# Optimization experiments

Measured on AMD Instinct MI355X. Metric: run time of the kernel, lower is better.

## Reference

```python
import jax, jax.numpy as jnp
import numpy as np

EPS = 1e-5  # torch default for InstanceNorm2d and BatchNorm2d
B, C, H, W = 16, 128, 8192, 1


def _instance_norm(x):
    # normalize over spatial dims (H, W) per sample, per channel; affine=False (torch default)
    mean = jnp.mean(x, axis=(2, 3), keepdims=True)
    var = jnp.var(x, axis=(2, 3), keepdims=True)
    return (x - mean) * jax.lax.rsqrt(var + EPS)


def _batch_norm(x, gamma, beta):
    # training-mode batch norm: stats over (B, H, W) per channel, affine transform
    mean = jnp.mean(x, axis=(0, 2, 3), keepdims=True)
    var = jnp.var(x, axis=(0, 2, 3), keepdims=True)
    xn = (x - mean) * jax.lax.rsqrt(var + EPS)
    return xn * gamma[None, :, None, None] + beta[None, :, None, None]


def _block(x, g, be, w, b):
    # InstanceNorm -> BatchNorm -> ReLU -> 1x1 Conv
    x = jax.nn.relu(_batch_norm(_instance_norm(x), g, be))
    return jnp.einsum('bchw,oc->bohw', x, w) + b[None, :, None, None]


def setup_inputs() -> dict:
    key = jax.random.key(0)
    ks = jax.random.split(key, 6)
    return {
        'Correlation_feats': jax.random.normal(ks[0], (B, C, H, W), jnp.float32),
        'Coherence_residual_feats': jax.random.normal(ks[1], (B, C, H, W), jnp.float32),
        'feats': jax.random.normal(ks[2], (B, C, H, W), jnp.float32),
        'fc_w': jax.random.normal(ks[3], (2 * C,), jnp.float32) * 0.05,
        'fc_b': jnp.zeros((1,), jnp.float32),
        'w1': jax.random.normal(ks[4], (C, C), jnp.float32) * (1.0 / np.sqrt(C)),
        'b1': jnp.zeros((C,), jnp.float32),
        'g1': jnp.ones((C,), jnp.float32),
        'be1': jnp.zeros((C,), jnp.float32),
        'w2': jax.random.normal(ks[5], (C, C), jnp.float32) * (1.0 / np.sqrt(C)),
        'b2': jnp.zeros((C,), jnp.float32),
        'g2': jnp.ones((C,), jnp.float32),
        'be2': jnp.zeros((C,), jnp.float32),
    }


def reference(Correlation_feats, Coherence_residual_feats, feats,
              fc_w, fc_b, w1, b1, g1, be1, w2, b2, g2, be2):
    # pre_defined_alpha is None branch: alpha = sigmoid(fc(cat(Corr, Coh)))
    cat = jnp.concatenate([Correlation_feats, Coherence_residual_feats], axis=1)  # [B,2C,H,W]
    logit = jnp.einsum('bchw,c->bhw', cat, fc_w)[:, None, :, :] + fc_b[0]  # [B,1,H,W]
    alpha = jax.nn.sigmoid(logit)
    agg = Correlation_feats - alpha * feats
    x = _block(agg, g1, be1, w1, b1)
    x = _block(x, g2, be2, w2, b2)
    return x
```

## Files before the change

### kernel.cpp

```cpp
#include <hip/hip_runtime.h>

#define NB 16
#define NC 128
#define NH 8192
#define EPSN 1e-5f

typedef __attribute__((ext_vector_type(8))) short short8;
typedef __attribute__((ext_vector_type(4))) float f32x4;

__device__ inline unsigned short f2bf(float f) {
  unsigned int u = __builtin_bit_cast(unsigned int, f);
  u = u + 0x7FFFu + ((u >> 16) & 1u);
  return (unsigned short)(u >> 16);
}
__device__ inline float bf2f(unsigned short h) {
  unsigned int u = ((unsigned int)h) << 16;
  return __builtin_bit_cast(float, u);
}

__global__ __launch_bounds__(256, 4) void alpha_kernel(
    const float* __restrict__ corr, const float* __restrict__ coh,
    const float* __restrict__ fcw, const float* __restrict__ fcb,
    float* __restrict__ alpha) {
  __shared__ float part[8][128];
  const int t = threadIdx.x;
  const int b = blockIdx.x >> 6;
  const int h0 = (blockIdx.x & 63) << 7;
  const int cg = t >> 5;
  const int quad = t & 31;

  const float* pc = corr + ((size_t)(b * NC + cg * 8) << 13) + h0 + quad * 4;
  const float* ph = coh + ((size_t)(b * NC + cg * 8) << 13) + h0 + quad * 4;

  float fw0[8], fw1[8], fw2[8], fw3[8];
#pragma unroll
  for (int k = 0; k < 2; ++k) {
    *(float4*)&fw0[k * 4] = *(const float4*)(fcw + cg * 8 + k * 4);
    *(float4*)&fw1[k * 4] = *(const float4*)(fcw + 64 + cg * 8 + k * 4);
    *(float4*)&fw2[k * 4] = *(const float4*)(fcw + 128 + cg * 8 + k * 4);
    *(float4*)&fw3[k * 4] = *(const float4*)(fcw + 192 + cg * 8 + k * 4);
  }

  float4 xa[8], xb[8], xc[8], xd[8];
#pragma unroll
  for (int j = 0; j < 8; ++j) xa[j] = *(const float4*)(pc + ((size_t)j << 13));
#pragma unroll
  for (int j = 0; j < 8; ++j)
    xb[j] = *(const float4*)(pc + ((size_t)(64 + j) << 13));

  float4 acc0 = {0, 0, 0, 0}, acc1 = {0, 0, 0, 0};
#pragma unroll
  for (int j = 0; j < 8; ++j) xc[j] = *(const float4*)(ph + ((size_t)j << 13));
#pragma unroll
  for (int j = 0; j < 8; ++j) {
    acc0.x = fmaf(xa[j].x, fw0[j], acc0.x);
    acc0.y = fmaf(xa[j].y, fw0[j], acc0.y);
    acc0.z = fmaf(xa[j].z, fw0[j], acc0.z);
    acc0.w = fmaf(xa[j].w, fw0[j], acc0.w);
  }
#pragma unroll
  for (int j = 0; j < 8; ++j)
    xd[j] = *(const float4*)(ph + ((size_t)(64 + j) << 13));
#pragma unroll
  for (int j = 0; j < 8; ++j) {
    acc1.x = fmaf(xb[j].x, fw1[j], acc1.x);
    acc1.y = fmaf(xb[j].y, fw1[j], acc1.y);
    acc1.z = fmaf(xb[j].z, fw1[j], acc1.z);
    acc1.w = fmaf(xb[j].w, fw1[j], acc1.w);
  }
#pragma unroll
  for (int j = 0; j < 8; ++j) {
    acc0.x = fmaf(xc[j].x, fw2[j], acc0.x);
    acc0.y = fmaf(xc[j].y, fw2[j], acc0.y);
    acc0.z = fmaf(xc[j].z, fw2[j], acc0.z);
    acc0.w = fmaf(xc[j].w, fw2[j], acc0.w);
  }
#pragma unroll
  for (int j = 0; j < 8; ++j) {
    acc1.x = fmaf(xd[j].x, fw3[j], acc1.x);
    acc1.y = fmaf(xd[j].y, fw3[j], acc1.y);
    acc1.z = fmaf(xd[j].z, fw3[j], acc1.z);
    acc1.w = fmaf(xd[j].w, fw3[j], acc1.w);
  }

  float4 s;
  s.x = acc0.x + acc1.x;
  s.y = acc0.y + acc1.y;
  s.z = acc0.z + acc1.z;
  s.w = acc0.w + acc1.w;
  *(float4*)&part[cg][quad * 4] = s;
  __syncthreads();
  if (t < 128) {
    float l = fcb[0];
#pragma unroll
    for (int pidx = 0; pidx < 8; ++pidx) l += part[pidx][t];
    alpha[b * NH + h0 + t] = 1.0f / (1.0f + __expf(-l));
  }
}

__global__ __launch_bounds__(256) void agg_kernel(
    const float* __restrict__ corr, const float* __restrict__ feats,
    const float* __restrict__ alpha, float* __restrict__ agg,
    float* __restrict__ stats) {
  int blk = blockIdx.x;
  int chunk = blk & 3;
  int bc = blk >> 2;
  int b = bc >> 7;
  size_t base = (size_t)bc * NH + chunk * 2048;
  const float* pa = alpha + (size_t)b * NH + chunk * 2048;
  int t = threadIdx.x;
  float s = 0.f, q = 0.f;
#pragma unroll
  for (int r = 0; r < 2; ++r) {
    int off = r * 1024 + t * 4;
    float4 cv = *(const float4*)(corr + base + off);
    float4 fv = *(const float4*)(feats + base + off);
    float4 av = *(const float4*)(pa + off);
    float4 g;
    g.x = cv.x - av.x * fv.x;
    g.y = cv.y - av.y * fv.y;
    g.z = cv.z - av.z * fv.z;
    g.w = cv.w - av.w * fv.w;
    *(float4*)(agg + base + off) = g;
    s += (g.x + g.y) + (g.z + g.w);
    q = fmaf(g.x, g.x, q);
    q = fmaf(g.y, g.y, q);
    q = fmaf(g.z, g.z, q);
    q = fmaf(g.w, g.w, q);
  }
#pragma unroll
  for (int m = 32; m >= 1; m >>= 1) {
    s += __shfl_xor(s, m);
    q += __shfl_xor(q, m);
  }
  __shared__ float red[8];
  int wid = t >> 6;
  if ((t & 63) == 0) {
    red[wid * 2] = s;
    red[wid * 2 + 1] = q;
  }
  __syncthreads();
  if (t == 0) {
    float S = (red[0] + red[2]) + (red[4] + red[6]);
    float Q = (red[1] + red[3]) + (red[5] + red[7]);
    atomicAdd(&stats[bc * 2], S);
    atomicAdd(&stats[bc * 2 + 1], Q);
  }
}

__global__ void finalize_kernel(const float* __restrict__ stats,
                                const float* __restrict__ g,
                                const float* __restrict__ be,
                                float* __restrict__ scale,
                                float* __restrict__ shift) {
  int c = threadIdx.x;
  float mean[NB], rstd[NB];
  float bnacc = 0.f;
#pragma unroll
  for (int b = 0; b < NB; ++b) {
    float s = stats[(b * NC + c) * 2];
    float q = stats[(b * NC + c) * 2 + 1];
    float m = s * (1.f / NH);
    float v = fmaxf(q * (1.f / NH) - m * m, 0.f);
    float r = rsqrtf(v + EPSN);
    mean[b] = m;
    rstd[b] = r;
    bnacc += v * r * r;
  }
  float bnr = rsqrtf(bnacc * (1.f / NB) + EPSN);
  float gc = g[c], bec = be[c];
#pragma unroll
  for (int b = 0; b < NB; ++b) {
    float sc = rstd[b] * bnr * gc;
    scale[b * NC + c] = sc;
    shift[b * NC + c] = fmaf(-mean[b], sc, bec);
  }
}

template <bool INBF, bool OUTBF, bool DOSTATS>
__global__ __launch_bounds__(256) void conv_mfma_kernel(
    const void* Xv, const float* __restrict__ scale,
    const float* __restrict__ shift, const float* __restrict__ W,
    const float* __restrict__ bias, void* Outv, float* __restrict__ stats) {
  __shared__ __align__(16) unsigned short sXf[8192];
  __shared__ float ssum[NC], ssq[NC];
  const int t = threadIdx.x;
  const int b = blockIdx.x >> 6;
  const int hbase = (blockIdx.x & 63) << 7;
  const int lane = t & 63;
  const int wv = t >> 6;
  const int wo = wv >> 1;
  const int wh = wv & 1;

  if (DOSTATS && t < NC) { ssum[t] = 0.f; ssq[t] = 0.f; }

  const int cb = (t >> 4) << 3;
  const int hq = t & 15;
  const int fragw = ((hq >> 2) << 2) + (cb >> 5);
  const int sub0 = (((cb >> 3) & 3) << 4) + ((hq & 3) << 2);
  const unsigned swz = ((unsigned)(sub0 >> 3)) << 4;
  const unsigned br = ((unsigned)(lane << 4)) ^ (((unsigned)(lane >> 3)) << 4);

  const float* Xf = (const float*)Xv;
  const unsigned short* Xh = (const unsigned short*)Xv;
  float* Of = (float*)Outv;
  unsigned short* Oh = (unsigned short*)Outv;

  float4 xv[8];
#pragma unroll
  for (int p = 0; p < 8; ++p) {
    size_t idx = ((size_t)(b * NC + cb + p) << 13) + hbase + hq * 4;
    if (INBF) {
      ushort4 u = *(const ushort4*)(Xh + idx);
      xv[p] = make_float4(bf2f(u.x), bf2f(u.y), bf2f(u.z), bf2f(u.w));
    } else {
      xv[p] = *(const float4*)(Xf + idx);
    }
  }

  float scv[8], shv[8];
#pragma unroll
  for (int p = 0; p < 8; ++p) {
    scv[p] = scale[b * NC + cb + p];
    shv[p] = shift[b * NC + cb + p];
  }

  short8 wfr[4][4];
  {
    const int orow = wo * 64 + (lane & 15);
    const int cbw = 8 * (lane >> 4);
#pragma unroll
    for (int m = 0; m < 4; ++m) {
#pragma unroll
      for (int k = 0; k < 4; ++k) {
        const float* p = W + (orow + m * 16) * NC + k * 32 + cbw;
        float4 lo = *(const float4*)p;
        float4 hi = *(const float4*)(p + 4);
        union { short8 s; unsigned short u[8]; } fr;
        fr.u[0] = f2bf(lo.x); fr.u[1] = f2bf(lo.y);
        fr.u[2] = f2bf(lo.z); fr.u[3] = f2bf(lo.w);
        fr.u[4] = f2bf(hi.x); fr.u[5] = f2bf(hi.y);
        fr.u[6] = f2bf(hi.z); fr.u[7] = f2bf(hi.w);
        wfr[m][k] = fr.s;
      }
    }
  }

  float as_[4][4], aq_[4][4];
  if (DOSTATS) {
#pragma unroll
    for (int m = 0; m < 4; ++m)
#pragma unroll
      for (int r = 0; r < 4; ++r) { as_[m][r] = 0.f; aq_[m][r] = 0.f; }
  }

  const int og = (lane >> 4) << 2;
  const int hcol = lane & 15;

  for (int tt = 0; tt < 2; ++tt) {
#pragma unroll
    for (int r = 0; r < 4; ++r) {
      union { short8 s; unsigned short u[8]; } pk;
#pragma unroll
      for (int p = 0; p < 8; ++p) {
        float v = (r == 0) ? xv[p].x : (r == 1) ? xv[p].y : (r == 2) ? xv[p].z : xv[p].w;
        pk.u[p] = f2bf(fmaxf(fmaf(v, scv[p], shv[p]), 0.f));
      }
      unsigned addr = ((unsigned)(fragw << 10)) + ((((unsigned)(sub0 + r)) << 4) ^ swz);
      *(short8*)((char*)sXf + addr) = pk.s;
    }
    if (tt < 1) {
#pragma unroll
      for (int p = 0; p < 8; ++p) {
        size_t idx = ((size_t)(b * NC + cb + p) << 13) + hbase + 64 + hq * 4;
        if (INBF) {
          ushort4 u = *(const ushort4*)(Xh + idx);
          xv[p] = make_float4(bf2f(u.x), bf2f(u.y), bf2f(u.z), bf2f(u.w));
        } else {
          xv[p] = *(const float4*)(Xf + idx);
        }
      }
    }
    __syncthreads();

    f32x4 acc[4][2];
#pragma unroll
    for (int m = 0; m < 4; ++m) {
      acc[m][0] = (f32x4){0.f, 0.f, 0.f, 0.f};
      acc[m][1] = (f32x4){0.f, 0.f, 0.f, 0.f};
    }
#pragma unroll
    for (int k = 0; k < 4; ++k) {
      short8 x0 = *(const short8*)((char*)sXf + (((wh * 2 + 0) * 4 + k) << 10) + br);
      short8 x1 = *(const short8*)((char*)sXf + (((wh * 2 + 1) * 4 + k) << 10) + br);
#pragma unroll
      for (int m = 0; m < 4; ++m) {
        acc[m][0] = __builtin_amdgcn_mfma_f32_16x16x32_bf16(wfr[m][k], x0, acc[m][0], 0, 0, 0);
        acc[m][1] = __builtin_amdgcn_mfma_f32_16x16x32_bf16(wfr[m][k], x1, acc[m][1], 0, 0, 0);
      }
    }

    const int ha = hbase + tt * 64 + wh * 32 + hcol;
#pragma unroll
    for (int m = 0; m < 4; ++m) {
      int obase = wo * 64 + m * 16 + og;
#pragma unroll
      for (int r = 0; r < 4; ++r) {
        int o = obase + r;
        float bv = bias[o];
        float v0 = acc[m][0][r] + bv;
        float v1 = acc[m][1][r] + bv;
        size_t ob = ((size_t)(b * NC + o) << 13);
        if (OUTBF) {
          Oh[ob + ha] = f2bf(v0);
          Oh[ob + ha + 16] = f2bf(v1);
        } else {
          Of[ob + ha] = v0;
          Of[ob + ha + 16] = v1;
        }
        if (DOSTATS) {
          as_[m][r] += v0 + v1;
          aq_[m][r] = fmaf(v0, v0, fmaf(v1, v1, aq_[m][r]));
        }
      }
    }
    __syncthreads();
  }

  if (DOSTATS) {
#pragma unroll
    for (int m = 0; m < 4; ++m) {
#pragma unroll
      for (int r = 0; r < 4; ++r) {
        float s = as_[m][r], q = aq_[m][r];
#pragma unroll
        for (int mm = 1; mm <= 8; mm <<= 1) {
          s += __shfl_xor(s, mm);
          q += __shfl_xor(q, mm);
        }
        if (hcol == 0) {
          int o = wo * 64 + m * 16 + og + r;
          atomicAdd(&ssum[o], s);
          atomicAdd(&ssq[o], q);
        }
      }
    }
    __syncthreads();
    if (t < NC) {
      atomicAdd(&stats[(b * NC + t) * 2], ssum[t]);
      atomicAdd(&stats[(b * NC + t) * 2 + 1], ssq[t]);
    }
  }
}

extern "C" void kernel_launch(void* const* d_in, const int* in_sizes, int n_in,
                              void* d_out, int out_size, void* d_ws,
                              size_t ws_size, hipStream_t stream) {
  const float* corr = (const float*)d_in[0];
  const float* coh = (const float*)d_in[1];
  const float* feats = (const float*)d_in[2];
  const float* fcw = (const float*)d_in[3];
  const float* fcb = (const float*)d_in[4];
  const float* w1 = (const float*)d_in[5];
  const float* b1 = (const float*)d_in[6];
  const float* g1 = (const float*)d_in[7];
  const float* be1 = (const float*)d_in[8];
  const float* w2 = (const float*)d_in[9];
  const float* b2 = (const float*)d_in[10];
  const float* g2 = (const float*)d_in[11];
  const float* be2 = (const float*)d_in[12];

  float* out = (float*)d_out;
  float* ws = (float*)d_ws;
  float* alphab = ws;
  float* stats1 = alphab + 131072;
  float* stats2 = stats1 + 4096;
  float* scale1 = stats2 + 4096;
  float* shift1 = scale1 + 2048;
  float* scale2 = shift1 + 2048;
  float* shift2 = scale2 + 2048;
  const size_t small_floats = 131072 + 4096 + 4096 + 4 * 2048;
  unsigned short* x1h = (unsigned short*)(ws + small_floats);
  const size_t need = small_floats * sizeof(float) +
                      (size_t)NB * NC * NH * sizeof(unsigned short);

  hipMemsetAsync(stats1, 0, 8192 * sizeof(float), stream);
  alpha_kernel<<<1024, 256, 0, stream>>>(corr, coh, fcw, fcb, alphab);
  agg_kernel<<<8192, 256, 0, stream>>>(corr, feats, alphab, out, stats1);
  finalize_kernel<<<1, 128, 0, stream>>>(stats1, g1, be1, scale1, shift1);

  if (ws_size >= need) {
    conv_mfma_kernel<false, true, true><<<1024, 256, 0, stream>>>(
        out, scale1, shift1, w1, b1, x1h, stats2);
    finalize_kernel<<<1, 128, 0, stream>>>(stats2, g2, be2, scale2, shift2);
    conv_mfma_kernel<true, false, false><<<1024, 256, 0, stream>>>(
        x1h, scale2, shift2, w2, b2, out, nullptr);
  } else {
    conv_mfma_kernel<false, false, true><<<1024, 256, 0, stream>>>(
        out, scale1, shift1, w1, b1, out, stats2);
    finalize_kernel<<<1, 128, 0, stream>>>(stats2, g2, be2, scale2, shift2);
    conv_mfma_kernel<false, false, false><<<1024, 256, 0, stream>>>(
        out, scale2, shift2, w2, b2, out, nullptr);
  }
}
```

Measured before the change: 132.7 us.

## Rewrite alpha kernel with double-buffered direct global-to-LDS channel loads

After: 143.9 us. +8.5%, slower.

```diff
diff --git a/kernel.cpp b/kernel.cpp
--- a/kernel.cpp
+++ b/kernel.cpp
@@ -18,84 +18,54 @@
   return __builtin_bit_cast(float, u);
 }
 
-__global__ __launch_bounds__(256, 4) void alpha_kernel(
+__global__ __launch_bounds__(256) void alpha_kernel(
     const float* __restrict__ corr, const float* __restrict__ coh,
     const float* __restrict__ fcw, const float* __restrict__ fcb,
     float* __restrict__ alpha) {
-  __shared__ float part[8][128];
+  __shared__ __align__(16) float sbuf[2][4096];
   const int t = threadIdx.x;
-  const int b = blockIdx.x >> 6;
-  const int h0 = (blockIdx.x & 63) << 7;
-  const int cg = t >> 5;
-  const int quad = t & 31;
-
-  const float* pc = corr + ((size_t)(b * NC + cg * 8) << 13) + h0 + quad * 4;
-  const float* ph = coh + ((size_t)(b * NC + cg * 8) << 13) + h0 + quad * 4;
-
-  float fw0[8], fw1[8], fw2[8], fw3[8];
-#pragma unroll
-  for (int k = 0; k < 2; ++k) {
-    *(float4*)&fw0[k * 4] = *(const float4*)(fcw + cg * 8 + k * 4);
-    *(float4*)&fw1[k * 4] = *(const float4*)(fcw + 64 + cg * 8 + k * 4);
-    *(float4*)&fw2[k * 4] = *(const float4*)(fcw + 128 + cg * 8 + k * 4);
-    *(float4*)&fw3[k * 4] = *(const float4*)(fcw + 192 + cg * 8 + k * 4);
-  }
-
-  float4 xa[8], xb[8], xc[8], xd[8];
-#pragma unroll
-  for (int j = 0; j < 8; ++j) xa[j] = *(const float4*)(pc + ((size_t)j << 13));
-#pragma unroll
-  for (int j = 0; j < 8; ++j)
-    xb[j] = *(const float4*)(pc + ((size_t)(64 + j) << 13));
-
-  float4 acc0 = {0, 0, 0, 0}, acc1 = {0, 0, 0, 0};
-#pragma unroll
-  for (int j = 0; j < 8; ++j) xc[j] = *(const float4*)(ph + ((size_t)j << 13));
-#pragma unroll
-  for (int j = 0; j < 8; ++j) {
-    acc0.x = fmaf(xa[j].x, fw0[j], acc0.x);
-    acc0.y = fmaf(xa[j].y, fw0[j], acc0.y);
-    acc0.z = fmaf(xa[j].z, fw0[j], acc0.z);
-    acc0.w = fmaf(xa[j].w, fw0[j], acc0.w);
-  }
-#pragma unroll
-  for (int j = 0; j < 8; ++j)
-    xd[j] = *(const float4*)(ph + ((size_t)(64 + j) << 13));
-#pragma unroll
-  for (int j = 0; j < 8; ++j) {
-    acc1.x = fmaf(xb[j].x, fw1[j], acc1.x);
-    acc1.y = fmaf(xb[j].y, fw1[j], acc1.y);
-    acc1.z = fmaf(xb[j].z, fw1[j], acc1.z);
-    acc1.w = fmaf(xb[j].w, fw1[j], acc1.w);
-  }
-#pragma unroll
-  for (int j = 0; j < 8; ++j) {
-    acc0.x = fmaf(xc[j].x, fw2[j], acc0.x);
-    acc0.y = fmaf(xc[j].y, fw2[j], acc0.y);
-    acc0.z = fmaf(xc[j].z, fw2[j], acc0.z);
-    acc0.w = fmaf(xc[j].w, fw2[j], acc0.w);
-  }
-#pragma unroll
-  for (int j = 0; j < 8; ++j) {
-    acc1.x = fmaf(xd[j].x, fw3[j], acc1.x);
-    acc1.y = fmaf(xd[j].y, fw3[j], acc1.y);
-    acc1.z = fmaf(xd[j].z, fw3[j], acc1.z);
-    acc1.w = fmaf(xd[j].w, fw3[j], acc1.w);
-  }
-
-  float4 s;
-  s.x = acc0.x + acc1.x;
-  s.y = acc0.y + acc1.y;
-  s.z = acc0.z + acc1.z;
-  s.w = acc0.w + acc1.w;
-  *(float4*)&part[cg][quad * 4] = s;
-  __syncthreads();
-  if (t < 128) {
-    float l = fcb[0];
-#pragma unroll
-    for (int pidx = 0; pidx < 8; ++pidx) l += part[pidx][t];
-    alpha[b * NH + h0 + t] = 1.0f / (1.0f + __expf(-l));
-  }
+  const int b = blockIdx.x >> 5;
+  const int h0 = (blockIdx.x & 31) << 8;
+  const int w = t >> 6;
+  const int lane = t & 63;
+
+#define STAGE(BUFIDX, K)                                                       \
+  {                                                                            \
+    const float* src_ = ((K) < 8) ? corr : coh;                                \
+    const float* g_ = src_ +                                                   \
+                      ((size_t)(b * NC + (((K) & 7) * 16) + 4 * w) << 13) +    \
+                      h0 + lane * 4;                                           \
+    _Pragma("unroll") for (int r_ = 0; r_ < 4; ++r_) {                         \
+      __builtin_amdgcn_global_load_lds(                                        \
+          (const __attribute__((address_space(1))) void*)(g_ +                 \
+                                                          ((size_t)r_ << 13)), \
+          (__attribute__((address_space(3))) void*)&sbuf[BUFIDX]               \
+                                                        [(4 * w + r_) * 256],  \
+          16, 0, 0);                                                           \
+    }                                                                          \
+  }
+
+  STAGE(0, 0);
+  float acc0 = 0.f, acc1 = 0.f;
+  for (int k = 0; k < 16; ++k) {
+    if (k < 15) STAGE((k + 1) & 1, k + 1);
+    __syncthreads();
+    float wreg[16];
+#pragma unroll
+    for (int q = 0; q < 4; ++q)
+      *(float4*)&wreg[q * 4] = *(const float4*)(fcw + k * 16 + q * 4);
+    const float* bufc = &sbuf[k & 1][0];
+#pragma unroll
+    for (int j = 0; j < 16; j += 2) {
+      acc0 = fmaf(bufc[j * 256 + t], wreg[j], acc0);
+      acc1 = fmaf(bufc[(j + 1) * 256 + t], wreg[j + 1], acc1);
+    }
+    __syncthreads();
+  }
+#undef STAGE
+
+  float l = acc0 + acc1 + fcb[0];
+  alpha[b * NH + h0 + t] = 1.0f / (1.0f + __expf(-l));
 }
 
 __global__ __launch_bounds__(256) void agg_kernel(
@@ -385,7 +355,7 @@
                       (size_t)NB * NC * NH * sizeof(unsigned short);
 
   hipMemsetAsync(stats1, 0, 8192 * sizeof(float), stream);
-  alpha_kernel<<<1024, 256, 0, stream>>>(corr, coh, fcw, fcb, alphab);
+  alpha_kernel<<<512, 256, 0, stream>>>(corr, coh, fcw, fcb, alphab);
   agg_kernel<<<8192, 256, 0, stream>>>(corr, feats, alphab, out, stats1);
   finalize_kernel<<<1, 128, 0, stream>>>(stats1, g1, be1, scale1, shift1);
 
```

## Split alpha logit computation into channel-partitioned partial sums plus reduction kernel

Applied to the files above, without the earlier changes.

Result: slower. 137.0 us (+3.3%).

```diff
diff --git a/kernel.cpp b/kernel.cpp
--- a/kernel.cpp
+++ b/kernel.cpp
@@ -18,7 +18,56 @@
   return __builtin_bit_cast(float, u);
 }
 
-__global__ __launch_bounds__(256, 4) void alpha_kernel(
+__global__ __launch_bounds__(256) void alpha_part_kernel(
+    const float* __restrict__ corr, const float* __restrict__ coh,
+    const float* __restrict__ fcw, float* __restrict__ partial) {
+  const int t = threadIdx.x;
+  const int blk = blockIdx.x;
+  const int pt = blk & 3;
+  const int cr = (blk >> 2) & 3;
+  const int src = (blk >> 4) & 1;
+  const int b = blk >> 5;
+  const float* X = src ? coh : corr;
+  const float* P = X + ((size_t)(b * NC + cr * 32) << 13) + pt * 2048 + t * 8;
+  const float* fw = fcw + src * NC + cr * 32;
+
+  float acc[8];
+#pragma unroll
+  for (int j = 0; j < 8; ++j) acc[j] = 0.f;
+#pragma unroll 4
+  for (int c = 0; c < 32; ++c) {
+    const float w = fw[c];
+    float4 v0 = *(const float4*)(P + ((size_t)c << 13));
+    float4 v1 = *(const float4*)(P + ((size_t)c << 13) + 4);
+    acc[0] = fmaf(v0.x, w, acc[0]);
+    acc[1] = fmaf(v0.y, w, acc[1]);
+    acc[2] = fmaf(v0.z, w, acc[2]);
+    acc[3] = fmaf(v0.w, w, acc[3]);
+    acc[4] = fmaf(v1.x, w, acc[4]);
+    acc[5] = fmaf(v1.y, w, acc[5]);
+    acc[6] = fmaf(v1.z, w, acc[6]);
+    acc[7] = fmaf(v1.w, w, acc[7]);
+  }
+  float* O = partial + (((size_t)(src * 4 + cr) * NB + b) << 13) + pt * 2048 +
+             t * 8;
+  *(float4*)O = make_float4(acc[0], acc[1], acc[2], acc[3]);
+  *(float4*)(O + 4) = make_float4(acc[4], acc[5], acc[6], acc[7]);
+}
+
+__global__ __launch_bounds__(256) void alpha_red_kernel(
+    const float* __restrict__ partial, const float* __restrict__ fcb,
+    float* __restrict__ alpha) {
+  const int i = blockIdx.x * 256 + threadIdx.x;
+  const int b = i >> 13;
+  const int px = i & (NH - 1);
+  float l = fcb[0];
+#pragma unroll
+  for (int p = 0; p < 8; ++p)
+    l += partial[(((size_t)p * NB + b) << 13) + px];
+  alpha[i] = 1.0f / (1.0f + __expf(-l));
+}
+
+__global__ __launch_bounds__(256, 4) void alpha_fb_kernel(
     const float* __restrict__ corr, const float* __restrict__ coh,
     const float* __restrict__ fcw, const float* __restrict__ fcb,
     float* __restrict__ alpha) {
@@ -28,10 +77,8 @@
   const int h0 = (blockIdx.x & 63) << 7;
   const int cg = t >> 5;
   const int quad = t & 31;
-
   const float* pc = corr + ((size_t)(b * NC + cg * 8) << 13) + h0 + quad * 4;
   const float* ph = coh + ((size_t)(b * NC + cg * 8) << 13) + h0 + quad * 4;
-
   float fw0[8], fw1[8], fw2[8], fw3[8];
 #pragma unroll
   for (int k = 0; k < 2; ++k) {
@@ -40,14 +87,12 @@
     *(float4*)&fw2[k * 4] = *(const float4*)(fcw + 128 + cg * 8 + k * 4);
     *(float4*)&fw3[k * 4] = *(const float4*)(fcw + 192 + cg * 8 + k * 4);
   }
-
   float4 xa[8], xb[8], xc[8], xd[8];
 #pragma unroll
   for (int j = 0; j < 8; ++j) xa[j] = *(const float4*)(pc + ((size_t)j << 13));
 #pragma unroll
   for (int j = 0; j < 8; ++j)
     xb[j] = *(const float4*)(pc + ((size_t)(64 + j) << 13));
-
   float4 acc0 = {0, 0, 0, 0}, acc1 = {0, 0, 0, 0};
 #pragma unroll
   for (int j = 0; j < 8; ++j) xc[j] = *(const float4*)(ph + ((size_t)j << 13));
@@ -82,7 +127,6 @@
     acc1.z = fmaf(xd[j].z, fw3[j], acc1.z);
     acc1.w = fmaf(xd[j].w, fw3[j], acc1.w);
   }
-
   float4 s;
   s.x = acc0.x + acc1.x;
   s.y = acc0.y + acc1.y;
@@ -380,16 +424,25 @@
   float* scale2 = shift1 + 2048;
   float* shift2 = scale2 + 2048;
   const size_t small_floats = 131072 + 4096 + 4096 + 4 * 2048;
-  unsigned short* x1h = (unsigned short*)(ws + small_floats);
-  const size_t need = small_floats * sizeof(float) +
-                      (size_t)NB * NC * NH * sizeof(unsigned short);
+  float* partial = ws + small_floats;
+  const size_t part_floats = 8 * NB * NH;
+  const size_t need_part = (small_floats + part_floats) * sizeof(float);
+  unsigned short* x1h = (unsigned short*)(partial + part_floats);
+  const size_t need_x1 =
+      need_part + (size_t)NB * NC * NH * sizeof(unsigned short);
 
   hipMemsetAsync(stats1, 0, 8192 * sizeof(float), stream);
-  alpha_kernel<<<1024, 256, 0, stream>>>(corr, coh, fcw, fcb, alphab);
+
+  if (ws_size >= need_part) {
+    alpha_part_kernel<<<512, 256, 0, stream>>>(corr, coh, fcw, partial);
+    alpha_red_kernel<<<512, 256, 0, stream>>>(partial, fcb, alphab);
+  } else {
+    alpha_fb_kernel<<<1024, 256, 0, stream>>>(corr, coh, fcw, fcb, alphab);
+  }
   agg_kernel<<<8192, 256, 0, stream>>>(corr, feats, alphab, out, stats1);
   finalize_kernel<<<1, 128, 0, stream>>>(stats1, g1, be1, scale1, shift1);
 
-  if (ws_size >= need) {
+  if (ws_size >= need_x1) {
     conv_mfma_kernel<false, true, true><<<1024, 256, 0, stream>>>(
         out, scale1, shift1, w1, b1, x1h, stats2);
     finalize_kernel<<<1, 128, 0, stream>>>(stats2, g2, be2, scale2, shift2);
```

## Split alpha projection into partial-sum and reduction kernels for more parallelism

Applied to the files above, without the earlier changes.

Result: slower. 139.8 us (+5.3%).

```diff
diff --git a/kernel.cpp b/kernel.cpp
--- a/kernel.cpp
+++ b/kernel.cpp
@@ -18,7 +18,71 @@
   return __builtin_bit_cast(float, u);
 }
 
-__global__ __launch_bounds__(256, 4) void alpha_kernel(
+__global__ __launch_bounds__(256) void alpha_part_kernel(
+    const float* __restrict__ corr, const float* __restrict__ coh,
+    const float* __restrict__ fcw, float* __restrict__ partial) {
+  const int t = threadIdx.x;
+  const int blk = blockIdx.x;
+  const int pt = blk & 7;
+  const int vg = (blk >> 3) & 31;
+  const int b = blk >> 8;
+  const int src = vg >> 4;
+  const int c0 = (vg & 15) << 3;
+  const float* X = src ? coh : corr;
+  const float* P = X + ((size_t)(b * NC + c0) << 13) + pt * 1024 + t * 4;
+  const float* fw = fcw + src * NC + c0;
+
+  float4 v[8];
+#pragma unroll
+  for (int j = 0; j < 8; ++j) v[j] = *(const float4*)(P + ((size_t)j << 13));
+  __builtin_amdgcn_sched_barrier(0);
+
+  float w[8];
+#pragma unroll
+  for (int j = 0; j < 8; ++j) w[j] = fw[j];
+
+  float4 a0 = {0, 0, 0, 0}, a1 = {0, 0, 0, 0};
+#pragma unroll
+  for (int j = 0; j < 8; j += 2) {
+    a0.x = fmaf(v[j].x, w[j], a0.x);
+    a0.y = fmaf(v[j].y, w[j], a0.y);
+    a0.z = fmaf(v[j].z, w[j], a0.z);
+    a0.w = fmaf(v[j].w, w[j], a0.w);
+    a1.x = fmaf(v[j + 1].x, w[j + 1], a1.x);
+    a1.y = fmaf(v[j + 1].y, w[j + 1], a1.y);
+    a1.z = fmaf(v[j + 1].z, w[j + 1], a1.z);
+    a1.w = fmaf(v[j + 1].w, w[j + 1], a1.w);
+  }
+  float4 s;
+  s.x = a0.x + a1.x;
+  s.y = a0.y + a1.y;
+  s.z = a0.z + a1.z;
+  s.w = a0.w + a1.w;
+  *(float4*)(partial + ((size_t)vg * NB * NH) + ((size_t)b << 13) + pt * 1024 +
+             t * 4) = s;
+}
+
+__global__ __launch_bounds__(256) void alpha_red_kernel(
+    const float* __restrict__ partial, const float* __restrict__ fcb,
+    float* __restrict__ alpha) {
+  const int i = blockIdx.x * 256 + threadIdx.x;
+  float p[32];
+#pragma unroll
+  for (int v = 0; v < 32; ++v) p[v] = partial[(size_t)v * NB * NH + i];
+  __builtin_amdgcn_sched_barrier(0);
+  float l0 = fcb[0], l1 = 0.f, l2 = 0.f, l3 = 0.f;
+#pragma unroll
+  for (int v = 0; v < 32; v += 4) {
+    l0 += p[v];
+    l1 += p[v + 1];
+    l2 += p[v + 2];
+    l3 += p[v + 3];
+  }
+  float l = (l0 + l1) + (l2 + l3);
+  alpha[i] = 1.0f / (1.0f + __expf(-l));
+}
+
+__global__ __launch_bounds__(256, 4) void alpha_fb_kernel(
     const float* __restrict__ corr, const float* __restrict__ coh,
     const float* __restrict__ fcw, const float* __restrict__ fcb,
     float* __restrict__ alpha) {
@@ -28,10 +92,8 @@
   const int h0 = (blockIdx.x & 63) << 7;
   const int cg = t >> 5;
   const int quad = t & 31;
-
   const float* pc = corr + ((size_t)(b * NC + cg * 8) << 13) + h0 + quad * 4;
   const float* ph = coh + ((size_t)(b * NC + cg * 8) << 13) + h0 + quad * 4;
-
   float fw0[8], fw1[8], fw2[8], fw3[8];
 #pragma unroll
   for (int k = 0; k < 2; ++k) {
@@ -40,14 +102,12 @@
     *(float4*)&fw2[k * 4] = *(const float4*)(fcw + 128 + cg * 8 + k * 4);
     *(float4*)&fw3[k * 4] = *(const float4*)(fcw + 192 + cg * 8 + k * 4);
   }
-
   float4 xa[8], xb[8], xc[8], xd[8];
 #pragma unroll
   for (int j = 0; j < 8; ++j) xa[j] = *(const float4*)(pc + ((size_t)j << 13));
 #pragma unroll
   for (int j = 0; j < 8; ++j)
     xb[j] = *(const float4*)(pc + ((size_t)(64 + j) << 13));
-
   float4 acc0 = {0, 0, 0, 0}, acc1 = {0, 0, 0, 0};
 #pragma unroll
   for (int j = 0; j < 8; ++j) xc[j] = *(const float4*)(ph + ((size_t)j << 13));
@@ -82,7 +142,6 @@
     acc1.z = fmaf(xd[j].z, fw3[j], acc1.z);
     acc1.w = fmaf(xd[j].w, fw3[j], acc1.w);
   }
-
   float4 s;
   s.x = acc0.x + acc1.x;
   s.y = acc0.y + acc1.y;
@@ -380,16 +439,26 @@
   float* scale2 = shift1 + 2048;
   float* shift2 = scale2 + 2048;
   const size_t small_floats = 131072 + 4096 + 4096 + 4 * 2048;
-  unsigned short* x1h = (unsigned short*)(ws + small_floats);
-  const size_t need = small_floats * sizeof(float) +
-                      (size_t)NB * NC * NH * sizeof(unsigned short);
+
+  float* partial = ws + small_floats;
+  unsigned short* x1h = (unsigned short*)partial;
+  const size_t part_floats = (size_t)32 * NB * NH;
+  const size_t need_part = (small_floats + part_floats) * sizeof(float);
+  const size_t need_x1 = small_floats * sizeof(float) +
+                         (size_t)NB * NC * NH * sizeof(unsigned short);
 
   hipMemsetAsync(stats1, 0, 8192 * sizeof(float), stream);
-  alpha_kernel<<<1024, 256, 0, stream>>>(corr, coh, fcw, fcb, alphab);
+
+  if (ws_size >= need_part) {
+    alpha_part_kernel<<<4096, 256, 0, stream>>>(corr, coh, fcw, partial);
+    alpha_red_kernel<<<512, 256, 0, stream>>>(partial, fcb, alphab);
+  } else {
+    alpha_fb_kernel<<<1024, 256, 0, stream>>>(corr, coh, fcw, fcb, alphab);
+  }
   agg_kernel<<<8192, 256, 0, stream>>>(corr, feats, alphab, out, stats1);
   finalize_kernel<<<1, 128, 0, stream>>>(stats1, g1, be1, scale1, shift1);
 
-  if (ws_size >= need) {
+  if (ws_size >= need_x1) {
     conv_mfma_kernel<false, true, true><<<1024, 256, 0, stream>>>(
         out, scale1, shift1, w1, b1, x1h, stats2);
     finalize_kernel<<<1, 128, 0, stream>>>(stats2, g2, be2, scale2, shift2);
```
